# Performance work log

Hardware: AMD Instinct MI355X
Metric: run time of the kernel (lower is better)

The kernel has to match this reference:

```python
import jax, jax.numpy as jnp
import numpy as np

N_Q = 4  # n_qubits == hidden_dim


def _qgate(z, phi):
    # Quantum circuit closed form: all gates are single-qubit RX, so the state is a
    # product state. Wires 0,1 get RX(z[:,w]) encoding then trainable RX(phi[w]);
    # wires >=2 get only trainable RX(phi[w]). <PauliZ> after RX(theta)|0> = cos(theta).
    B = z.shape[0]
    ang01 = z[:, :2] + phi[:2]                                  # [B, 2]
    ang_rest = jnp.broadcast_to(phi[2:], (B, N_Q - 2))          # [B, N_Q-2]
    return jnp.cos(jnp.concatenate([ang01, ang_rest], axis=1))  # [B, N_Q]


def setup_inputs() -> dict:
    key = jax.random.key(0)
    ks = jax.random.split(key, 13)
    T, B, D, H = 512, 256, 256, N_Q
    s = 0.1
    inp = {"inputs": jax.random.normal(ks[0], (T, B, D), dtype=jnp.float32)}
    for j, n in enumerate(["f", "i", "u", "o"]):
        inp["W" + n] = jax.random.normal(ks[1 + 3 * j], (H, D + H), dtype=jnp.float32) * s
        inp["b" + n] = jax.random.normal(ks[2 + 3 * j], (H,), dtype=jnp.float32) * s
        inp["phi_" + n] = jax.random.normal(ks[3 + 3 * j], (H,), dtype=jnp.float32) * s
    return inp


def reference(inputs, Wf, bf, phi_f, Wi, bi, phi_i, Wu, bu, phi_u, Wo, bo, phi_o):
    B = inputs.shape[1]
    H = Wf.shape[0]

    def step(carry, x):
        hx, cx = carry
        c = jnp.concatenate([x, hx], axis=1)                     # [B, D+H]
        f = jax.nn.sigmoid(_qgate(c @ Wf.T + bf, phi_f))
        i = jax.nn.sigmoid(_qgate(c @ Wi.T + bi, phi_i))
        g = jnp.tanh(_qgate(c @ Wu.T + bu, phi_u))
        o = jax.nn.sigmoid(_qgate(c @ Wo.T + bo, phi_o))
        cx_new = f * cx + i * g
        hx_new = o * jnp.tanh(cx_new)
        return (hx_new, cx_new), hx_new

    h0 = jnp.zeros((B, H), inputs.dtype)
    c0 = jnp.zeros((B, H), inputs.dtype)
    (hx, cx), outputs = jax.lax.scan(step, (h0, c0), inputs)
    return outputs, hx, cx
```

## Files before the change

### kernel.cpp

```cpp
#include <hip/hip_runtime.h>
#include <math.h>

#define TT 512
#define BB 256
#define DD 256
#define ROWS (TT * BB)
#define INV2PI 0.15915494309189535f

typedef float v2f __attribute__((ext_vector_type(2)));
typedef float v4f __attribute__((ext_vector_type(4)));
typedef short s8v __attribute__((ext_vector_type(8)));

__device__ __forceinline__ v2f pkfma(v2f a, v2f b, v2f c) {
    return __builtin_elementwise_fma(a, b, c);
}
__device__ __forceinline__ v2f cos2(v2f a) {
    v2f r;
    r.x = __builtin_amdgcn_cosf(a.x);
    r.y = __builtin_amdgcn_cosf(a.y);
    return r;
}
__device__ __forceinline__ v2f sig2(v2f x) {
    v2f u = x * x;
    v2f p = pkfma(u, (v2f)(-2.1081349e-4f), (v2f)(2.0833333e-3f));
    p = pkfma(u, p, (v2f)(-2.0833333e-2f));
    p = pkfma(u, p, (v2f)(0.25f));
    return pkfma(x, p, (v2f)(0.5f));
}
__device__ __forceinline__ v2f tanh2(v2f x) {
    v2f u = x * x;
    v2f n = pkfma(u + (v2f)(105.0f), u, (v2f)(945.0f));
    v2f d = pkfma(pkfma(u, (v2f)(15.0f), (v2f)(420.0f)), u, (v2f)(945.0f));
    v2f r;
    r.x = __builtin_amdgcn_rcpf(d.x);
    r.y = __builtin_amdgcn_rcpf(d.y);
    return x * n * r;
}

__device__ __forceinline__ uint32_t bfr(float f) {
    uint32_t b = __float_as_uint(f);
    return b + 0x7FFFu + ((b >> 16) & 1u);
}
__device__ __forceinline__ uint32_t packbf(float lo, float hi) {
    return (bfr(hi) & 0xFFFF0000u) | (bfr(lo) >> 16);
}
__device__ __forceinline__ s8v pack8(v4f lo, v4f hi) {
    union { uint32_t u[4]; s8v s; } r;
    r.u[0] = packbf(lo.x, lo.y);
    r.u[1] = packbf(lo.z, lo.w);
    r.u[2] = packbf(hi.x, hi.y);
    r.u[3] = packbf(hi.z, hi.w);
    return r.s;
}

__global__ __launch_bounds__(256) void qlstm_table(
    const float* __restrict__ Wf, const float* __restrict__ bf, const float* __restrict__ pf,
    const float* __restrict__ Wi, const float* __restrict__ bi, const float* __restrict__ pi,
    const float* __restrict__ Wu, const float* __restrict__ bu, const float* __restrict__ pu,
    const float* __restrict__ Wo, const float* __restrict__ bo, const float* __restrict__ po,
    float* __restrict__ hcf_g, float* __restrict__ hob_g) {
    const int tid = threadIdx.x;
    const float* Ws[4] = {Wf, Wi, Wu, Wo};
    const float* Bs[4] = {bf, bi, bu, bo};
    const float* Ps[4] = {pf, pi, pu, po};

    float l2fc[2], Scc[2], occ[2], ricc[2];
#pragma unroll
    for (int w = 0; w < 2; ++w) {
        const int q = w + 2;
        float fv = 1.0f / (1.0f + expf(-cosf(Ps[0][q])));
        float iv = 1.0f / (1.0f + expf(-cosf(Ps[1][q])));
        float gv = tanhf(cosf(Ps[2][q]));
        float ov = 1.0f / (1.0f + expf(-cosf(Ps[3][q])));
        l2fc[w] = log2f(fv);
        Scc[w] = iv * gv;
        occ[w] = ov;
        ricc[w] = 1.0f / (1.0f - fv);
    }
    float bb[8];
#pragma unroll
    for (int g = 0; g < 4; ++g)
#pragma unroll
        for (int wire = 0; wire < 2; ++wire) bb[g * 2 + wire] = Bs[g][wire] + Ps[g][wire];

    for (int t = tid; t < TT; t += 256) {
        float h2 = occ[0] * tanhf(Scc[0] * (1.0f - exp2f((float)t * l2fc[0])) * ricc[0]);
        float h3 = occ[1] * tanhf(Scc[1] * (1.0f - exp2f((float)t * l2fc[1])) * ricc[1]);
        float ho2 = occ[0] * tanhf(Scc[0] * (1.0f - exp2f((float)(t + 1) * l2fc[0])) * ricc[0]);
        float ho3 = occ[1] * tanhf(Scc[1] * (1.0f - exp2f((float)(t + 1) * l2fc[1])) * ricc[1]);
#pragma unroll
        for (int g = 0; g < 4; ++g)
#pragma unroll
            for (int wire = 0; wire < 2; ++wire)
                hcf_g[t * 8 + g * 2 + wire] =
                    (bb[g * 2 + wire] + h2 * Ws[g][wire * 260 + 258] + h3 * Ws[g][wire * 260 + 259]) * INV2PI;
        hob_g[t * 2] = ho2;
        hob_g[t * 2 + 1] = ho3;
    }
}

__global__ __launch_bounds__(256) void qlstm_gemm(
    const float* __restrict__ x,
    const float* __restrict__ Wf, const float* __restrict__ Wi,
    const float* __restrict__ Wu, const float* __restrict__ Wo,
    const float* __restrict__ hcf_g, const float* __restrict__ hob_g,
    float* __restrict__ Z, float* __restrict__ out) {
    const int tid = threadIdx.x;
    const int lane = tid & 63;
    const int tile = blockIdx.x * 4 + (tid >> 6);
    const int rbase = tile * 16;
    const int t = tile >> 4;
    const int m = lane & 15;
    const int q = lane >> 4;
    const float* Ws[4] = {Wf, Wi, Wu, Wo};

    const int j = m & 7;
    const float* wrow = Ws[j >> 1] + (j & 1) * 260 + q * 8;
    s8v bfrag[8];
#pragma unroll
    for (int kk = 0; kk < 8; ++kk) {
        v4f wlo = *(const v4f*)(wrow + kk * 32);
        v4f whi = *(const v4f*)(wrow + kk * 32 + 4);
        bfrag[kk] = pack8(wlo, whi);
    }

    const float* xrow = x + (size_t)(rbase + m) * DD + q * 8;
    v4f acc = {0.f, 0.f, 0.f, 0.f};
#pragma unroll
    for (int kk = 0; kk < 8; ++kk) {
        v4f xlo = *(const v4f*)(xrow + kk * 32);
        v4f xhi = *(const v4f*)(xrow + kk * 32 + 4);
        s8v afrag = pack8(xlo, xhi);
        acc = __builtin_amdgcn_mfma_f32_16x16x32_bf16(afrag, bfrag[kk], acc, 0, 0, 0);
    }

    const float hc = hcf_g[t * 8 + j];
    if (m < 8) {
#pragma unroll
        for (int r = 0; r < 4; ++r) {
            const int row = rbase + q * 4 + r;
            Z[(size_t)row * 8 + m] = acc[r] * INV2PI + hc;
        }
    }
    if (lane >= 48) {
        const int row = rbase + (lane - 48);
        *(float2*)(out + (size_t)row * 4 + 2) = *(const float2*)&hob_g[t * 2];
    }
}

struct Ch {
    v2f h, c;
    v4f zb[4][2];
    int tw, t0;
};

__device__ __forceinline__ void ch_init(Ch& ch, const float* Zb, int tw, int t0) {
    ch.h = (v2f)(0.f);
    ch.c = (v2f)(0.f);
    ch.tw = tw;
    ch.t0 = t0;
#pragma unroll
    for (int s = 0; s < 4; ++s) {
        ch.zb[s][0] = *(const v4f*)(Zb + (size_t)(tw + s) * 2048);
        ch.zb[s][1] = *(const v4f*)(Zb + (size_t)(tw + s) * 2048 + 4);
    }
}

__device__ __forceinline__ void ch_step(Ch& ch, int s, int slot, const float* Zb,
                                        float* outp, const v2f* wa, const v2f* wb) {
    const int t = ch.tw + s;
    v4f zA = ch.zb[slot][0], zB = ch.zb[slot][1];
    int tp = t + 4;
    tp = (tp < TT) ? tp : (TT - 1);
    ch.zb[slot][0] = *(const v4f*)(Zb + (size_t)tp * 2048);
    ch.zb[slot][1] = *(const v4f*)(Zb + (size_t)tp * 2048 + 4);
    v2f zf = {zA.x, zA.y}, zi = {zA.z, zA.w}, zu = {zB.x, zB.y}, zo = {zB.z, zB.w};
    v2f h0s = (v2f)(ch.h.x), h1s = (v2f)(ch.h.y);
    v2f af = pkfma(h0s, wa[0], pkfma(h1s, wb[0], zf));
    v2f ai = pkfma(h0s, wa[1], pkfma(h1s, wb[1], zi));
    v2f au = pkfma(h0s, wa[2], pkfma(h1s, wb[2], zu));
    v2f ao = pkfma(h0s, wa[3], pkfma(h1s, wb[3], zo));
    v2f f = sig2(cos2(af));
    v2f i = sig2(cos2(ai));
    v2f g = tanh2(cos2(au));
    v2f o = sig2(cos2(ao));
    ch.c = pkfma(f, ch.c, i * g);
    ch.h = o * tanh2(ch.c);
    if (t >= ch.t0)
        *(v2f*)(outp + (size_t)t * 1024) = ch.h;
}

__global__ __launch_bounds__(64) void qlstm_scan(
    const float* __restrict__ Z,
    const float* __restrict__ Wf, const float* __restrict__ pf,
    const float* __restrict__ Wi, const float* __restrict__ pi,
    const float* __restrict__ Wu, const float* __restrict__ pu,
    const float* __restrict__ Wo, const float* __restrict__ po,
    float* __restrict__ out) {
    const int tid = threadIdx.x;
    const int cpair = blockIdx.x >> 2;
    const int b = (blockIdx.x & 3) * 64 + tid;
    const float* Ws[4] = {Wf, Wi, Wu, Wo};
    const float* Ps[4] = {pf, pi, pu, po};

    float cd[2], hd[2];
#pragma unroll
    for (int w = 0; w < 2; ++w) {
        const int q = w + 2;
        float fv = 1.0f / (1.0f + expf(-cosf(Ps[0][q])));
        float iv = 1.0f / (1.0f + expf(-cosf(Ps[1][q])));
        float gv = tanhf(cosf(Ps[2][q]));
        float ov = 1.0f / (1.0f + expf(-cosf(Ps[3][q])));
        float l2f = log2f(fv);
        float S = iv * gv;
        float ric = 1.0f / (1.0f - fv);
        cd[w] = S * (1.0f - exp2f(512.0f * l2f)) * ric;
        hd[w] = ov * tanhf(cd[w]);
    }

    v2f wa[4], wb[4];
#pragma unroll
    for (int g = 0; g < 4; ++g) {
        wa[g].x = Ws[g][256] * INV2PI;
        wa[g].y = Ws[g][260 + 256] * INV2PI;
        wb[g].x = Ws[g][257] * INV2PI;
        wb[g].y = Ws[g][260 + 257] * INV2PI;
    }

    const int t0A = cpair * 32;
    const int twA = (t0A >= 40) ? t0A - 40 : 0;
    const int lenA = t0A + 32 - twA;
    const int preA = 72 - lenA;
    const int t0B = (cpair + 8) * 32;
    const int twB = t0B - 40;

    const float* Zb = Z + (size_t)b * 8;
    float* outp = out + (size_t)b * 4;

    Ch A, B;
    ch_init(A, Zb, twA, t0A);
    ch_init(B, Zb, twB, t0B);

#pragma unroll 4
    for (int s = 0; s < preA; ++s)
        ch_step(B, s, s & 3, Zb, outp, wa, wb);
#pragma unroll 4
    for (int s = 0; s < lenA; ++s) {
        ch_step(A, s, s & 3, Zb, outp, wa, wb);
        ch_step(B, preA + s, s & 3, Zb, outp, wa, wb);
    }

    if (cpair == 7) {
        *(float4*)(out + (size_t)TT * BB * 4 + (size_t)b * 4) =
            make_float4(B.h.x, B.h.y, hd[0], hd[1]);
        *(float4*)(out + (size_t)TT * BB * 4 + (size_t)BB * 4 + (size_t)b * 4) =
            make_float4(B.c.x, B.c.y, cd[0], cd[1]);
    }
}

extern "C" void kernel_launch(void* const* d_in, const int* in_sizes, int n_in,
                              void* d_out, int out_size, void* d_ws, size_t ws_size,
                              hipStream_t stream) {
    (void)in_sizes; (void)n_in; (void)out_size; (void)ws_size;
    const float* x  = (const float*)d_in[0];
    const float* Wf = (const float*)d_in[1];
    const float* bf = (const float*)d_in[2];
    const float* pf = (const float*)d_in[3];
    const float* Wi = (const float*)d_in[4];
    const float* bi = (const float*)d_in[5];
    const float* pi = (const float*)d_in[6];
    const float* Wu = (const float*)d_in[7];
    const float* bu = (const float*)d_in[8];
    const float* pu = (const float*)d_in[9];
    const float* Wo = (const float*)d_in[10];
    const float* bo = (const float*)d_in[11];
    const float* po = (const float*)d_in[12];
    float* out = (float*)d_out;
    float* Z = (float*)d_ws;
    float* hcf_g = Z + (size_t)ROWS * 8;
    float* hob_g = hcf_g + TT * 8;

    qlstm_table<<<1, 256, 0, stream>>>(Wf, bf, pf, Wi, bi, pi, Wu, bu, pu,
                                       Wo, bo, po, hcf_g, hob_g);
    qlstm_gemm<<<2048, 256, 0, stream>>>(x, Wf, Wi, Wu, Wo, hcf_g, hob_g, Z, out);
    qlstm_scan<<<32, 64, 0, stream>>>(Z, Wf, pf, Wi, pi, Wu, pu, Wo, po, out);
}
```

Measured before the change: 252.5 us.

## Replace bf16 MFMA projection with fp32 dot products and shuffle-tree reduction

The input-projection GEMM drops the bf16 MFMA path, which packed x and W into bf16 fragments. Each wave now handles one row at a time, taking 16 rows strided by 8192. Each lane computes fp32 partial dot products over 4 columns for all 8 gate-wire outputs. A transpose-style butterfly shuffle then reduces the 8 values across the wave. This removes the bf16 conversion work and keeps full fp32 precision, but the FMAs move from matrix cores to vector ALUs and add many cross-lane shuffles per row. The kernel is likely bandwidth-bound on reading x, so the main effect depends on whether loads stay coalesced.

```diff
diff --git a/kernel.cpp b/kernel.cpp
--- a/kernel.cpp
+++ b/kernel.cpp
@@ -9,7 +9,6 @@
 
 typedef float v2f __attribute__((ext_vector_type(2)));
 typedef float v4f __attribute__((ext_vector_type(4)));
-typedef short s8v __attribute__((ext_vector_type(8)));
 
 __device__ __forceinline__ v2f pkfma(v2f a, v2f b, v2f c) {
     return __builtin_elementwise_fma(a, b, c);
@@ -37,20 +36,31 @@
     return x * n * r;
 }
 
-__device__ __forceinline__ uint32_t bfr(float f) {
-    uint32_t b = __float_as_uint(f);
-    return b + 0x7FFFu + ((b >> 16) & 1u);
-}
-__device__ __forceinline__ uint32_t packbf(float lo, float hi) {
-    return (bfr(hi) & 0xFFFF0000u) | (bfr(lo) >> 16);
-}
-__device__ __forceinline__ s8v pack8(v4f lo, v4f hi) {
-    union { uint32_t u[4]; s8v s; } r;
-    r.u[0] = packbf(lo.x, lo.y);
-    r.u[1] = packbf(lo.z, lo.w);
-    r.u[2] = packbf(hi.x, hi.y);
-    r.u[3] = packbf(hi.z, hi.w);
-    return r.s;
+__device__ __forceinline__ float reduce8(float p[8], int lane) {
+    const bool b0 = lane & 1;
+#pragma unroll
+    for (int k = 0; k < 4; ++k) {
+        float send = b0 ? p[k] : p[k + 4];
+        float q = __shfl_xor(send, 1, 64);
+        p[k] = (b0 ? p[k + 4] : p[k]) + q;
+    }
+    const bool b1 = lane & 2;
+#pragma unroll
+    for (int k = 0; k < 2; ++k) {
+        float send = b1 ? p[k] : p[k + 2];
+        float q = __shfl_xor(send, 2, 64);
+        p[k] = (b1 ? p[k + 2] : p[k]) + q;
+    }
+    const bool b2 = lane & 4;
+    {
+        float send = b2 ? p[0] : p[1];
+        float q = __shfl_xor(send, 4, 64);
+        p[0] = (b2 ? p[1] : p[0]) + q;
+    }
+    p[0] += __shfl_xor(p[0], 8, 64);
+    p[0] += __shfl_xor(p[0], 16, 64);
+    p[0] += __shfl_xor(p[0], 32, 64);
+    return p[0];
 }
 
 __global__ __launch_bounds__(256) void qlstm_table(
@@ -107,44 +117,44 @@
     float* __restrict__ Z, float* __restrict__ out) {
     const int tid = threadIdx.x;
     const int lane = tid & 63;
-    const int tile = blockIdx.x * 4 + (tid >> 6);
-    const int rbase = tile * 16;
-    const int t = tile >> 4;
-    const int m = lane & 15;
-    const int q = lane >> 4;
+    const int wid = (blockIdx.x * 256 + tid) >> 6;
     const float* Ws[4] = {Wf, Wi, Wu, Wo};
 
-    const int j = m & 7;
-    const float* wrow = Ws[j >> 1] + (j & 1) * 260 + q * 8;
-    s8v bfrag[8];
-#pragma unroll
-    for (int kk = 0; kk < 8; ++kk) {
-        v4f wlo = *(const v4f*)(wrow + kk * 32);
-        v4f whi = *(const v4f*)(wrow + kk * 32 + 4);
-        bfrag[kk] = pack8(wlo, whi);
-    }
-
-    const float* xrow = x + (size_t)(rbase + m) * DD + q * 8;
-    v4f acc = {0.f, 0.f, 0.f, 0.f};
-#pragma unroll
-    for (int kk = 0; kk < 8; ++kk) {
-        v4f xlo = *(const v4f*)(xrow + kk * 32);
-        v4f xhi = *(const v4f*)(xrow + kk * 32 + 4);
-        s8v afrag = pack8(xlo, xhi);
-        acc = __builtin_amdgcn_mfma_f32_16x16x32_bf16(afrag, bfrag[kk], acc, 0, 0, 0);
-    }
-
-    const float hc = hcf_g[t * 8 + j];
-    if (m < 8) {
-#pragma unroll
-        for (int r = 0; r < 4; ++r) {
-            const int row = rbase + q * 4 + r;
-            Z[(size_t)row * 8 + m] = acc[r] * INV2PI + hc;
+    float4 wv[8];
+#pragma unroll
+    for (int g = 0; g < 4; ++g)
+#pragma unroll
+        for (int wire = 0; wire < 2; ++wire)
+            wv[g * 2 + wire] = *(const float4*)(Ws[g] + wire * 260 + 4 * lane);
+    const int v = ((lane & 1) << 2) | (lane & 2) | ((lane >> 2) & 1);
+
+#pragma unroll
+    for (int k = 0; k < 16; k += 4) {
+        v4f xv[4];
+#pragma unroll
+        for (int j = 0; j < 4; ++j) {
+            const int r = wid + (k + j) * 8192;
+            xv[j] = *(const v4f*)(x + (size_t)r * DD + 4 * lane);
         }
-    }
-    if (lane >= 48) {
-        const int row = rbase + (lane - 48);
-        *(float2*)(out + (size_t)row * 4 + 2) = *(const float2*)&hob_g[t * 2];
+        float s[4];
+#pragma unroll
+        for (int j = 0; j < 4; ++j) {
+            float p[8];
+#pragma unroll
+            for (int m = 0; m < 8; ++m)
+                p[m] = xv[j].x * wv[m].x + xv[j].y * wv[m].y + xv[j].z * wv[m].z + xv[j].w * wv[m].w;
+            s[j] = reduce8(p, lane);
+        }
+        if (lane < 8) {
+#pragma unroll
+            for (int j = 0; j < 4; ++j) {
+                const int r = wid + (k + j) * 8192;
+                Z[(size_t)r * 8 + v] = s[j] * INV2PI + hcf_g[((r >> 8) << 3) + v];
+            }
+        } else if (lane < 12) {
+            const int r = wid + (k + lane - 8) * 8192;
+            *(float2*)(out + (size_t)r * 4 + 2) = *(const float2*)&hob_g[(r >> 8) * 2];
+        }
     }
 }
 
```

New measurement: 250.2 us. No clear change (-0.9%).
